# Optimization experiments

Measured on AMD Instinct MI355X. Metric: run time of the kernel, lower is better.

Reference implementation:

```python
import jax, jax.numpy as jnp
import numpy as np

N_NODES = 100000
N_EDGES = 3200000
D_IN = 128
D_OUT = 128


def setup_inputs() -> dict:
    key = jax.random.key(0)
    k1, k2, k3, k4, k5, k6 = jax.random.split(key, 6)
    features = jax.random.normal(k1, (N_NODES, D_IN), dtype=jnp.float32)
    norm = jax.random.uniform(k2, (N_EDGES, 1), dtype=jnp.float32)
    src = jax.random.randint(k3, (N_EDGES,), 0, N_NODES)
    dst = jax.random.randint(k4, (N_EDGES,), 0, N_NODES)
    weight = jax.random.normal(k5, (D_OUT, D_IN), dtype=jnp.float32) * (1.0 / np.sqrt(D_IN))
    bias = jax.random.normal(k6, (D_OUT,), dtype=jnp.float32) * 0.01
    return {"features": features, "norm": norm, "src": src, "dst": dst,
            "weight": weight, "bias": bias}


def reference(features, norm, src, dst, weight, bias):
    # message: per-edge gather of src features scaled by edge norm  [E, D_IN]
    msg = norm * features[src]
    # reduce: segment-sum into destination nodes  [N, D_IN]
    h_neigh = jax.ops.segment_sum(msg, dst, num_segments=N_NODES)
    # dense linear (nn.Linear: x @ W^T + b)  [N, D_OUT]
    return h_neigh @ weight.T + bias
```

## Files before the change

### kernel.cpp

```cpp
#include <hip/hip_runtime.h>


#define NN    100000
#define NE    3200000
#define D     128
#define NBKT2 1563
#define NTILE 6250

typedef __attribute__((ext_vector_type(8))) short bf16x8;
typedef __attribute__((ext_vector_type(4))) float f32x4;

static __device__ __forceinline__ unsigned short f2bf(float x) {
  unsigned u = __float_as_uint(x);
  u += 0x7FFFu + ((u >> 16) & 1u);
  return (unsigned short)(u >> 16);
}

static __device__ __forceinline__ void fmix8(float* acc, uint4 q, float nr) {
  asm("v_fma_mix_f32 %0, %1, %2, %0 op_sel:[0,0,0] op_sel_hi:[1,0,0]"
      : "+v"(acc[0]) : "v"(q.x), "v"(nr));
  asm("v_fma_mix_f32 %0, %1, %2, %0 op_sel:[1,0,0] op_sel_hi:[1,0,0]"
      : "+v"(acc[1]) : "v"(q.x), "v"(nr));
  asm("v_fma_mix_f32 %0, %1, %2, %0 op_sel:[0,0,0] op_sel_hi:[1,0,0]"
      : "+v"(acc[2]) : "v"(q.y), "v"(nr));
  asm("v_fma_mix_f32 %0, %1, %2, %0 op_sel:[1,0,0] op_sel_hi:[1,0,0]"
      : "+v"(acc[3]) : "v"(q.y), "v"(nr));
  asm("v_fma_mix_f32 %0, %1, %2, %0 op_sel:[0,0,0] op_sel_hi:[1,0,0]"
      : "+v"(acc[4]) : "v"(q.z), "v"(nr));
  asm("v_fma_mix_f32 %0, %1, %2, %0 op_sel:[1,0,0] op_sel_hi:[1,0,0]"
      : "+v"(acc[5]) : "v"(q.z), "v"(nr));
  asm("v_fma_mix_f32 %0, %1, %2, %0 op_sel:[0,0,0] op_sel_hi:[1,0,0]"
      : "+v"(acc[6]) : "v"(q.w), "v"(nr));
  asm("v_fma_mix_f32 %0, %1, %2, %0 op_sel:[1,0,0] op_sel_hi:[1,0,0]"
      : "+v"(acc[7]) : "v"(q.w), "v"(nr));
}

__global__ __launch_bounds__(256) void cvtw_kernel(
    const float* __restrict__ w, unsigned short* __restrict__ wfrag) {
  const int i = blockIdx.x * 256 + threadIdx.x;
  const int c = i >> 7, k = i & 127;
  const int pos = ((((c >> 4) << 2) + (k >> 5)) * 64 +
                   (((k >> 3) & 3) << 4) + (c & 15)) * 8 + (k & 7);
  wfrag[pos] = f2bf(w[i]);
}

__global__ __launch_bounds__(256) void gemm_kernel(
    const float* __restrict__ f, const unsigned short* __restrict__ wfrag,
    unsigned short* __restrict__ gh) {
  const int wv = blockIdx.x * 4 + (threadIdx.x >> 6);
  if (wv >= NTILE) return;
  const int lane = threadIdx.x & 63;
  const int mrow = lane & 15;
  const int q = lane >> 4;
  const long node = (long)wv * 16 + mrow;
  const float* fr = f + node * D + q * 8;

  bf16x8 a[4];
#pragma unroll
  for (int ks = 0; ks < 4; ++ks) {
    const float4 lo = *(const float4*)(fr + ks * 32);
    const float4 hi = *(const float4*)(fr + ks * 32 + 4);
    union { bf16x8 v; unsigned short u[8]; } pa;
    pa.u[0] = f2bf(lo.x); pa.u[1] = f2bf(lo.y);
    pa.u[2] = f2bf(lo.z); pa.u[3] = f2bf(lo.w);
    pa.u[4] = f2bf(hi.x); pa.u[5] = f2bf(hi.y);
    pa.u[6] = f2bf(hi.z); pa.u[7] = f2bf(hi.w);
    a[ks] = pa.v;
  }

  const long nbase = (long)wv * 16 + (q << 2);
#pragma unroll
  for (int tc = 0; tc < 8; ++tc) {
    f32x4 acc = {0.f, 0.f, 0.f, 0.f};
#pragma unroll
    for (int ks = 0; ks < 4; ++ks) {
      const bf16x8 b =
          *(const bf16x8*)(wfrag + (((tc << 2) + ks) * 64 + lane) * 8);
      acc = __builtin_amdgcn_mfma_f32_16x16x32_bf16(a[ks], b, acc, 0, 0, 0);
    }
    const int c = (tc << 4) + mrow;
#pragma unroll
    for (int r = 0; r < 4; ++r) {
      union { _Float16 h; unsigned short u; } cv;
      cv.h = (_Float16)acc[r];
      gh[(nbase + r) * D + c] = cv.u;
    }
  }
}

__global__ __launch_bounds__(256) void hist_kernel(const int* __restrict__ dst,
                                                   int* __restrict__ gcnt) {
  __shared__ int h[NBKT2];
  const int t = threadIdx.x;
  for (int b = t; b < NBKT2; b += 256) h[b] = 0;
  __syncthreads();
  const int base = blockIdx.x * 4096;
#pragma unroll
  for (int i = 0; i < 16; ++i) {
    int e = base + i * 256 + t;
    if (e < NE) atomicAdd(&h[dst[e] >> 6], 1);
  }
  __syncthreads();
  for (int b = t; b < NBKT2; b += 256)
    if (h[b]) atomicAdd(&gcnt[b], h[b]);
}

__global__ __launch_bounds__(1024) void scan_kernel(const int* __restrict__ gcnt,
                                                    int* __restrict__ bstart,
                                                    int* __restrict__ cur,
                                                    int* __restrict__ row_ptr) {
  __shared__ int s[2048];
  const int t = threadIdx.x;
  s[t] = (t < NBKT2) ? gcnt[t] : 0;
  s[t + 1024] = (t + 1024 < NBKT2) ? gcnt[t + 1024] : 0;
  __syncthreads();
  if (t < 64) {
    int part = 0;
#pragma unroll
    for (int i = 0; i < 32; ++i) part += s[(t << 5) + i];
    int inc = part;
#pragma unroll
    for (int off = 1; off < 64; off <<= 1) {
      int x = __shfl_up(inc, off, 64);
      if (t >= off) inc += x;
    }
    int run = inc - part;
#pragma unroll
    for (int i = 0; i < 32; ++i) {
      int idx = (t << 5) + i;
      int v = s[idx];
      s[idx] = run;
      run += v;
    }
  }
  __syncthreads();
  if (t < NBKT2) { bstart[t] = s[t]; cur[t] = s[t]; }
  if (t + 1024 < NBKT2) { bstart[t + 1024] = s[t + 1024]; cur[t + 1024] = s[t + 1024]; }
  if (t == 0) { bstart[NBKT2] = NE; row_ptr[NN] = NE; }
}

__global__ __launch_bounds__(512) void bin_kernel(
    const int* __restrict__ src, const int* __restrict__ dst,
    const float* __restrict__ norm, int* __restrict__ cur,
    int2* __restrict__ bufA) {
  __shared__ int bcnt[NBKT2];
  __shared__ int bbase[NBKT2];
  const int t = threadIdx.x;
  for (int b = t; b < NBKT2; b += 512) bcnt[b] = 0;
  __syncthreads();
  const int base = blockIdx.x * 16384;
#pragma unroll
  for (int i = 0; i < 32; ++i) {
    int e = base + i * 512 + t;
    if (e < NE) atomicAdd(&bcnt[dst[e] >> 6], 1);
  }
  __syncthreads();
  for (int b = t; b < NBKT2; b += 512) {
    int c = bcnt[b];
    if (c) bbase[b] = atomicAdd(&cur[b], c);
    bcnt[b] = 0;
  }
  __syncthreads();
#pragma unroll
  for (int i = 0; i < 32; ++i) {
    int e = base + i * 512 + t;
    if (e < NE) {
      int d = dst[e];
      int b = d >> 6;
      int r = atomicAdd(&bcnt[b], 1);
      int2 m;
      m.x = src[e] | ((d & 63) << 24);
      m.y = __float_as_int(norm[e]);
      bufA[bbase[b] + r] = m;
    }
  }
}

__global__ __launch_bounds__(256) void sort_kernel(
    const int2* __restrict__ bufA, const int* __restrict__ bstart,
    int2* __restrict__ bufB, int* __restrict__ row_ptr) {
  __shared__ int lcnt[64];
  __shared__ int lbase[64];
  const int b = blockIdx.x;
  const int t = threadIdx.x;
  const int beg = bstart[b];
  const int end = bstart[b + 1];
  if (t < 64) lcnt[t] = 0;
  __syncthreads();
  for (int e = beg + t; e < end; e += 256) {
    int2 m = bufA[e];
    atomicAdd(&lcnt[(m.x >> 24) & 63], 1);
  }
  __syncthreads();
  if (t < 64) {
    int v = lcnt[t];
    int inc = v;
#pragma unroll
    for (int off = 1; off < 64; off <<= 1) {
      int x = __shfl_up(inc, off, 64);
      if (t >= off) inc += x;
    }
    int ex = inc - v;
    lbase[t] = ex;
    int n = (b << 6) + t;
    if (n < NN) row_ptr[n] = beg + ex;
    lcnt[t] = 0;
  }
  __syncthreads();
  for (int e = beg + t; e < end; e += 256) {
    int2 m = bufA[e];
    int nl = (m.x >> 24) & 63;
    int r = atomicAdd(&lcnt[nl], 1);
    int2 o;
    o.x = m.x & 0xFFFFFF;
    o.y = m.y;
    bufB[beg + lbase[nl] + r] = o;
  }
}

__global__ __launch_bounds__(256) void pull_kernel(
    const unsigned short* __restrict__ gh, const int* __restrict__ row_ptr,
    const int2* __restrict__ bufB, const float* __restrict__ bias,
    float* __restrict__ out) {
  const int n = blockIdx.x * 4 + (threadIdx.x >> 6);
  if (n >= NN) return;
  const int lane = threadIdx.x & 63;
  const int s = lane & 15;
  const int g = lane >> 4;
  const int beg = row_ptr[n];
  const int end = row_ptr[n + 1];

  float acc[8] = {0.f, 0.f, 0.f, 0.f, 0.f, 0.f, 0.f, 0.f};

  if (beg < end) {
    const char* gbase = (const char*)gh;
    const unsigned soff = (unsigned)(s << 4);
    const int last = end - 1;
    int e0 = beg;
    int2 mA0 = bufB[min(e0 + g, last)];
    int2 mB0 = bufB[min(e0 + 4 + g, last)];
    uint4 qA0 = *(const uint4*)(gbase + (((unsigned)mA0.x << 8) + soff));
    uint4 qB0 = *(const uint4*)(gbase + (((unsigned)mB0.x << 8) + soff));
    int2 mA1 = bufB[min(e0 + 8 + g, last)];
    int2 mB1 = bufB[min(e0 + 12 + g, last)];
    while (e0 + 8 < end) {
      const int2 mA2 = bufB[min(e0 + 16 + g, last)];
      const int2 mB2 = bufB[min(e0 + 20 + g, last)];
      const uint4 qA1 =
          *(const uint4*)(gbase + (((unsigned)mA1.x << 8) + soff));
      const uint4 qB1 =
          *(const uint4*)(gbase + (((unsigned)mB1.x << 8) + soff));
      fmix8(acc, qA0, __int_as_float(mA0.y));
      fmix8(acc, qB0, __int_as_float(mB0.y));
      mA0 = mA1; mB0 = mB1;
      mA1 = mA2; mB1 = mB2;
      qA0 = qA1; qB0 = qB1;
      e0 += 8;
    }
    const float nrA = (e0 + g < end) ? __int_as_float(mA0.y) : 0.f;
    const float nrB = (e0 + 4 + g < end) ? __int_as_float(mB0.y) : 0.f;
    fmix8(acc, qA0, nrA);
    fmix8(acc, qB0, nrB);
  }

#pragma unroll
  for (int k = 0; k < 8; ++k) {
    acc[k] += __shfl_xor(acc[k], 16, 64);
    acc[k] += __shfl_xor(acc[k], 32, 64);
  }
  if (g < 2) {
    const bool hi = (g == 1);
    const float r0 = hi ? acc[4] : acc[0];
    const float r1 = hi ? acc[5] : acc[1];
    const float r2 = hi ? acc[6] : acc[2];
    const float r3 = hi ? acc[7] : acc[3];
    const int cb = (s << 3) + (g << 2);
    const float4 b4 = *(const float4*)(bias + cb);
    float4 r;
    r.x = r0 + b4.x;
    r.y = r1 + b4.y;
    r.z = r2 + b4.z;
    r.w = r3 + b4.w;
    *(float4*)(out + (long)n * D + cb) = r;
  }
}

__global__ __launch_bounds__(256) void gemm_f32_kernel(
    const float* __restrict__ f, const float* __restrict__ w,
    float* __restrict__ g) {
  __shared__ float wlds[D * D];
  const int t = threadIdx.x;
  for (int i = t; i < D * D; i += 256) {
    int c = i >> 7, k = i & 127;
    wlds[(c << 7) + (k ^ (c & 31))] = w[i];
  }
  __syncthreads();
  const int c = t & 127;
  const int cx = c & 31;
  const int cbase = c << 7;
  const int jbase = __builtin_amdgcn_readfirstlane((t >> 7) << 3);
  const long nb = (long)blockIdx.x * 16 + jbase;
  const float* __restrict__ frow = f + nb * D;
  float acc[8] = {0.f, 0.f, 0.f, 0.f, 0.f, 0.f, 0.f, 0.f};
#pragma unroll 4
  for (int k = 0; k < D; ++k) {
    float wv = wlds[cbase + (k ^ cx)];
#pragma unroll
    for (int j = 0; j < 8; ++j) acc[j] += frow[j * D + k] * wv;
  }
#pragma unroll
  for (int j = 0; j < 8; ++j) g[(nb + j) * D + c] = acc[j];
}

__global__ __launch_bounds__(256) void init_kernel(
    const float* __restrict__ bias, float4* __restrict__ out) {
  const int i = blockIdx.x * 256 + threadIdx.x;
  const float4* b4 = (const float4*)bias;
  out[i] = b4[i & 31];
}

__global__ __launch_bounds__(256) void scatter_kernel(
    const float* __restrict__ g, const float* __restrict__ norm,
    const int* __restrict__ src, const int* __restrict__ dst,
    float* __restrict__ out) {
  const long tid = (long)blockIdx.x * 256 + threadIdx.x;
  const int e = (int)(tid >> 5);
  if (e >= NE) return;
  const int ch = (int)(tid & 31) << 2;
  const int s = src[e];
  const int d = dst[e];
  const float nr = norm[e];
  const float4 gv = *(const float4*)(g + (long)s * D + ch);
  float* op = out + (long)d * D + ch;
  unsafeAtomicAdd(op + 0, nr * gv.x);
  unsafeAtomicAdd(op + 1, nr * gv.y);
  unsafeAtomicAdd(op + 2, nr * gv.z);
  unsafeAtomicAdd(op + 3, nr * gv.w);
}

extern "C" void kernel_launch(void* const* d_in, const int* in_sizes, int n_in,
                              void* d_out, int out_size, void* d_ws,
                              size_t ws_size, hipStream_t stream) {
  const float* features = (const float*)d_in[0];
  const float* norm     = (const float*)d_in[1];
  const int*   src      = (const int*)d_in[2];
  const int*   dst      = (const int*)d_in[3];
  const float* weight   = (const float*)d_in[4];
  const float* bias     = (const float*)d_in[5];
  float* out = (float*)d_out;

  char* ws = (char*)d_ws;
  unsigned short* gh    = (unsigned short*)ws;
  int2* bufA    = (int2*)(ws + 25600000);
  int2* bufB    = (int2*)(ws + 51200000);
  int*  row_ptr = (int*)(ws + 76800000);
  int*  gcnt    = (int*)(ws + 77200008);
  int*  bstart  = (int*)(ws + 77206264);
  int*  cur     = (int*)(ws + 77212524);
  unsigned short* wfrag = (unsigned short*)(ws + 77218784);
  const size_t need = 77251552;

  if (ws_size >= need) {
    hipMemsetAsync(gcnt, 0, NBKT2 * sizeof(int), stream);
    hipLaunchKernelGGL(cvtw_kernel, dim3(64), dim3(256), 0, stream,
                       weight, wfrag);
    hipLaunchKernelGGL(gemm_kernel, dim3((NTILE + 3) / 4), dim3(256), 0,
                       stream, features, wfrag, gh);
    hipLaunchKernelGGL(hist_kernel, dim3((NE + 4095) / 4096), dim3(256), 0,
                       stream, dst, gcnt);
    hipLaunchKernelGGL(scan_kernel, dim3(1), dim3(1024), 0, stream,
                       gcnt, bstart, cur, row_ptr);
    hipLaunchKernelGGL(bin_kernel, dim3((NE + 16383) / 16384), dim3(512), 0,
                       stream, src, dst, norm, cur, bufA);
    hipLaunchKernelGGL(sort_kernel, dim3(NBKT2), dim3(256), 0, stream,
                       bufA, bstart, bufB, row_ptr);
    hipLaunchKernelGGL(pull_kernel, dim3((NN + 3) / 4), dim3(256), 0, stream,
                       gh, row_ptr, bufB, bias, out);
  } else {
    float* g = (float*)ws;
    hipLaunchKernelGGL(gemm_f32_kernel, dim3(NN / 16), dim3(256), 0, stream,
                       features, weight, g);
    hipLaunchKernelGGL(init_kernel, dim3((NN * D / 4) / 256), dim3(256), 0,
                       stream, bias, (float4*)out);
    hipLaunchKernelGGL(scatter_kernel, dim3((long)NE * 32 / 256), dim3(256), 0,
                       stream, g, norm, src, dst, out);
  }
}
```

Before: 392.7 us.

## Replace two-level bucket sort with direct per-node counting sort via global atomics

Swaps the bucketed histogram, bin and local-sort pipeline for a per-node histogram built with global atomics, a single-block 100k-entry scan, and a placement kernel that scatters each edge straight to its final CSR slot using an atomic on its destination counter. This drops the intermediate bufA pass and the sort kernel, cutting memory traffic and kernel launches. In exchange it relies on heavy global atomic contention, scatters 8-byte writes at random addresses, and makes the order of edges within a node nondeterministic. The scan now runs on one block over 100k entries, which may serialize.

```diff
diff --git a/kernel.cpp b/kernel.cpp
--- a/kernel.cpp
+++ b/kernel.cpp
@@ -4,7 +4,6 @@
 #define NN    100000
 #define NE    3200000
 #define D     128
-#define NBKT2 1563
 #define NTILE 6250
 
 typedef __attribute__((ext_vector_type(8))) short bf16x8;
@@ -88,134 +87,105 @@
   }
 }
 
-__global__ __launch_bounds__(256) void hist_kernel(const int* __restrict__ dst,
-                                                   int* __restrict__ gcnt) {
-  __shared__ int h[NBKT2];
+__global__ __launch_bounds__(256) void histn_kernel(const int* __restrict__ dst,
+                                                    int* __restrict__ cur) {
+  const int i = blockIdx.x * 256 + threadIdx.x;
+  const int4 d = ((const int4*)dst)[i];
+  atomicAdd(&cur[d.x], 1);
+  atomicAdd(&cur[d.y], 1);
+  atomicAdd(&cur[d.z], 1);
+  atomicAdd(&cur[d.w], 1);
+}
+
+__global__ __launch_bounds__(1024) void scan100k_kernel(
+    int* __restrict__ cur, int* __restrict__ row_ptr) {
+  __shared__ int wsum[16];
   const int t = threadIdx.x;
-  for (int b = t; b < NBKT2; b += 256) h[b] = 0;
+  const int w = t >> 6, lane = t & 63;
+  const int wbeg = w * 6400;
+
+  int tot = 0;
+  for (int base = wbeg; base < wbeg + 6400; base += 256) {
+    const int idx = base + lane * 4;
+    int4 v = {0, 0, 0, 0};
+    if (idx + 3 < NN) v = *(const int4*)(cur + idx);
+    else {
+      if (idx + 0 < NN) v.x = cur[idx + 0];
+      if (idx + 1 < NN) v.y = cur[idx + 1];
+      if (idx + 2 < NN) v.z = cur[idx + 2];
+      if (idx + 3 < NN) v.w = cur[idx + 3];
+    }
+    tot += v.x + v.y + v.z + v.w;
+  }
+#pragma unroll
+  for (int off = 1; off < 64; off <<= 1) tot += __shfl_xor(tot, off, 64);
+  if (lane == 0) wsum[w] = tot;
   __syncthreads();
-  const int base = blockIdx.x * 4096;
-#pragma unroll
-  for (int i = 0; i < 16; ++i) {
-    int e = base + i * 256 + t;
-    if (e < NE) atomicAdd(&h[dst[e] >> 6], 1);
+  if (w == 0 && lane < 16) {
+    const int v = wsum[lane];
+    int inc = v;
+#pragma unroll
+    for (int off = 1; off < 16; off <<= 1) {
+      int x = __shfl_up(inc, off, 64);
+      if (lane >= off) inc += x;
+    }
+    wsum[lane] = inc - v;
   }
   __syncthreads();
-  for (int b = t; b < NBKT2; b += 256)
-    if (h[b]) atomicAdd(&gcnt[b], h[b]);
-}
-
-__global__ __launch_bounds__(1024) void scan_kernel(const int* __restrict__ gcnt,
-                                                    int* __restrict__ bstart,
-                                                    int* __restrict__ cur,
-                                                    int* __restrict__ row_ptr) {
-  __shared__ int s[2048];
-  const int t = threadIdx.x;
-  s[t] = (t < NBKT2) ? gcnt[t] : 0;
-  s[t + 1024] = (t + 1024 < NBKT2) ? gcnt[t + 1024] : 0;
-  __syncthreads();
-  if (t < 64) {
-    int part = 0;
-#pragma unroll
-    for (int i = 0; i < 32; ++i) part += s[(t << 5) + i];
-    int inc = part;
+
+  int run = wsum[w];
+  for (int base = wbeg; base < wbeg + 6400; base += 256) {
+    const int idx = base + lane * 4;
+    int4 v = {0, 0, 0, 0};
+    const bool full = (idx + 3 < NN);
+    if (full) v = *(const int4*)(cur + idx);
+    else {
+      if (idx + 0 < NN) v.x = cur[idx + 0];
+      if (idx + 1 < NN) v.y = cur[idx + 1];
+      if (idx + 2 < NN) v.z = cur[idx + 2];
+      if (idx + 3 < NN) v.w = cur[idx + 3];
+    }
+    const int s = v.x + v.y + v.z + v.w;
+    int inc = s;
 #pragma unroll
     for (int off = 1; off < 64; off <<= 1) {
       int x = __shfl_up(inc, off, 64);
-      if (t >= off) inc += x;
-    }
-    int run = inc - part;
-#pragma unroll
-    for (int i = 0; i < 32; ++i) {
-      int idx = (t << 5) + i;
-      int v = s[idx];
-      s[idx] = run;
-      run += v;
-    }
-  }
-  __syncthreads();
-  if (t < NBKT2) { bstart[t] = s[t]; cur[t] = s[t]; }
-  if (t + 1024 < NBKT2) { bstart[t + 1024] = s[t + 1024]; cur[t + 1024] = s[t + 1024]; }
-  if (t == 0) { bstart[NBKT2] = NE; row_ptr[NN] = NE; }
-}
-
-__global__ __launch_bounds__(512) void bin_kernel(
+      if (lane >= off) inc += x;
+    }
+    const int ex = run + inc - s;
+    int4 o;
+    o.x = ex;
+    o.y = ex + v.x;
+    o.z = ex + v.x + v.y;
+    o.w = ex + v.x + v.y + v.z;
+    if (full) {
+      *(int4*)(cur + idx) = o;
+      *(int4*)(row_ptr + idx) = o;
+    } else {
+      if (idx + 0 < NN) { cur[idx + 0] = o.x; row_ptr[idx + 0] = o.x; }
+      if (idx + 1 < NN) { cur[idx + 1] = o.y; row_ptr[idx + 1] = o.y; }
+      if (idx + 2 < NN) { cur[idx + 2] = o.z; row_ptr[idx + 2] = o.z; }
+      if (idx + 3 < NN) { cur[idx + 3] = o.w; row_ptr[idx + 3] = o.w; }
+    }
+    run += __shfl(inc, 63, 64);
+  }
+  if (t == 0) row_ptr[NN] = NE;
+}
+
+__global__ __launch_bounds__(256) void place_kernel(
     const int* __restrict__ src, const int* __restrict__ dst,
     const float* __restrict__ norm, int* __restrict__ cur,
-    int2* __restrict__ bufA) {
-  __shared__ int bcnt[NBKT2];
-  __shared__ int bbase[NBKT2];
-  const int t = threadIdx.x;
-  for (int b = t; b < NBKT2; b += 512) bcnt[b] = 0;
-  __syncthreads();
-  const int base = blockIdx.x * 16384;
-#pragma unroll
-  for (int i = 0; i < 32; ++i) {
-    int e = base + i * 512 + t;
-    if (e < NE) atomicAdd(&bcnt[dst[e] >> 6], 1);
-  }
-  __syncthreads();
-  for (int b = t; b < NBKT2; b += 512) {
-    int c = bcnt[b];
-    if (c) bbase[b] = atomicAdd(&cur[b], c);
-    bcnt[b] = 0;
-  }
-  __syncthreads();
-#pragma unroll
-  for (int i = 0; i < 32; ++i) {
-    int e = base + i * 512 + t;
-    if (e < NE) {
-      int d = dst[e];
-      int b = d >> 6;
-      int r = atomicAdd(&bcnt[b], 1);
-      int2 m;
-      m.x = src[e] | ((d & 63) << 24);
-      m.y = __float_as_int(norm[e]);
-      bufA[bbase[b] + r] = m;
-    }
-  }
-}
-
-__global__ __launch_bounds__(256) void sort_kernel(
-    const int2* __restrict__ bufA, const int* __restrict__ bstart,
-    int2* __restrict__ bufB, int* __restrict__ row_ptr) {
-  __shared__ int lcnt[64];
-  __shared__ int lbase[64];
-  const int b = blockIdx.x;
-  const int t = threadIdx.x;
-  const int beg = bstart[b];
-  const int end = bstart[b + 1];
-  if (t < 64) lcnt[t] = 0;
-  __syncthreads();
-  for (int e = beg + t; e < end; e += 256) {
-    int2 m = bufA[e];
-    atomicAdd(&lcnt[(m.x >> 24) & 63], 1);
-  }
-  __syncthreads();
-  if (t < 64) {
-    int v = lcnt[t];
-    int inc = v;
-#pragma unroll
-    for (int off = 1; off < 64; off <<= 1) {
-      int x = __shfl_up(inc, off, 64);
-      if (t >= off) inc += x;
-    }
-    int ex = inc - v;
-    lbase[t] = ex;
-    int n = (b << 6) + t;
-    if (n < NN) row_ptr[n] = beg + ex;
-    lcnt[t] = 0;
-  }
-  __syncthreads();
-  for (int e = beg + t; e < end; e += 256) {
-    int2 m = bufA[e];
-    int nl = (m.x >> 24) & 63;
-    int r = atomicAdd(&lcnt[nl], 1);
-    int2 o;
-    o.x = m.x & 0xFFFFFF;
-    o.y = m.y;
-    bufB[beg + lbase[nl] + r] = o;
-  }
+    int2* __restrict__ bufB) {
+  const int i = blockIdx.x * 256 + threadIdx.x;
+  const int4 s = ((const int4*)src)[i];
+  const int4 d = ((const int4*)dst)[i];
+  const float4 nr = ((const float4*)norm)[i];
+  int2 m;
+  int r;
+  r = atomicAdd(&cur[d.x], 1); m.x = s.x; m.y = __float_as_int(nr.x); bufB[r] = m;
+  r = atomicAdd(&cur[d.y], 1); m.x = s.y; m.y = __float_as_int(nr.y); bufB[r] = m;
+  r = atomicAdd(&cur[d.z], 1); m.x = s.z; m.y = __float_as_int(nr.z); bufB[r] = m;
+  r = atomicAdd(&cur[d.w], 1); m.x = s.w; m.y = __float_as_int(nr.w); bufB[r] = m;
 }
 
 __global__ __launch_bounds__(256) void pull_kernel(
@@ -351,29 +321,24 @@
 
   char* ws = (char*)d_ws;
   unsigned short* gh    = (unsigned short*)ws;
-  int2* bufA    = (int2*)(ws + 25600000);
-  int2* bufB    = (int2*)(ws + 51200000);
-  int*  row_ptr = (int*)(ws + 76800000);
-  int*  gcnt    = (int*)(ws + 77200008);
-  int*  bstart  = (int*)(ws + 77206264);
-  int*  cur     = (int*)(ws + 77212524);
-  unsigned short* wfrag = (unsigned short*)(ws + 77218784);
-  const size_t need = 77251552;
+  int2* bufB    = (int2*)(ws + 25600000);
+  int*  row_ptr = (int*)(ws + 51200000);
+  int*  cur     = (int*)(ws + 51600016);
+  unsigned short* wfrag = (unsigned short*)(ws + 52000016);
+  const size_t need = 52032784;
 
   if (ws_size >= need) {
-    hipMemsetAsync(gcnt, 0, NBKT2 * sizeof(int), stream);
+    hipMemsetAsync(cur, 0, NN * sizeof(int), stream);
     hipLaunchKernelGGL(cvtw_kernel, dim3(64), dim3(256), 0, stream,
                        weight, wfrag);
     hipLaunchKernelGGL(gemm_kernel, dim3((NTILE + 3) / 4), dim3(256), 0,
                        stream, features, wfrag, gh);
-    hipLaunchKernelGGL(hist_kernel, dim3((NE + 4095) / 4096), dim3(256), 0,
-                       stream, dst, gcnt);
-    hipLaunchKernelGGL(scan_kernel, dim3(1), dim3(1024), 0, stream,
-                       gcnt, bstart, cur, row_ptr);
-    hipLaunchKernelGGL(bin_kernel, dim3((NE + 16383) / 16384), dim3(512), 0,
-                       stream, src, dst, norm, cur, bufA);
-    hipLaunchKernelGGL(sort_kernel, dim3(NBKT2), dim3(256), 0, stream,
-                       bufA, bstart, bufB, row_ptr);
+    hipLaunchKernelGGL(histn_kernel, dim3(NE / 1024), dim3(256), 0, stream,
+                       dst, cur);
+    hipLaunchKernelGGL(scan100k_kernel, dim3(1), dim3(1024), 0, stream,
+                       cur, row_ptr);
+    hipLaunchKernelGGL(place_kernel, dim3(NE / 1024), dim3(256), 0, stream,
+                       src, dst, norm, cur, bufB);
     hipLaunchKernelGGL(pull_kernel, dim3((NN + 3) / 4), dim3(256), 0, stream,
                        gh, row_ptr, bufB, bias, out);
   } else {
```

New measurement: 628.9 us. 1.6x slower.

## Fuse histogram into GEMM launch and coarsen counting-sort buckets to 256 nodes

Applied to the files above, without the earlier changes.

Folds the destination histogram into the GEMM kernel as extra blocks so it runs concurrently with the feature transform. Bucket width grows from 64 to 256 nodes, which cuts the bucket count to 391, and the histogram and binning kernels read inputs as int4 with replicated shared-memory counters to reduce atomic contention. The sort kernel now handles 256 nodes per bucket with a two-level scan. Larger buckets mean fewer global atomics and launches, but the sort blocks become larger and less balanced.

```diff
diff --git a/kernel.cpp b/kernel.cpp
--- a/kernel.cpp
+++ b/kernel.cpp
@@ -4,8 +4,11 @@
 #define NN    100000
 #define NE    3200000
 #define D     128
-#define NBKT2 1563
+#define NBKT  391
+#define NI4   800000
 #define NTILE 6250
+#define GB    1563
+#define HB    782
 
 typedef __attribute__((ext_vector_type(8))) short bf16x8;
 typedef __attribute__((ext_vector_type(4))) float f32x4;
@@ -44,9 +47,36 @@
   wfrag[pos] = f2bf(w[i]);
 }
 
-__global__ __launch_bounds__(256) void gemm_kernel(
+__global__ __launch_bounds__(256) void gemmhist_kernel(
     const float* __restrict__ f, const unsigned short* __restrict__ wfrag,
-    unsigned short* __restrict__ gh) {
+    unsigned short* __restrict__ gh, const int* __restrict__ dst,
+    int* __restrict__ gcnt) {
+  __shared__ int h[4][NBKT];
+  if (blockIdx.x >= GB) {
+    const int t = threadIdx.x;
+    for (int i = t; i < 4 * NBKT; i += 256) ((int*)h)[i] = 0;
+    __syncthreads();
+    const int i4base = (blockIdx.x - GB) * 1024;
+    const int rep = t & 3;
+#pragma unroll
+    for (int i = 0; i < 4; ++i) {
+      const int idx = i4base + i * 256 + t;
+      if (idx < NI4) {
+        const int4 d = ((const int4*)dst)[idx];
+        atomicAdd(&h[rep][d.x >> 8], 1);
+        atomicAdd(&h[rep][d.y >> 8], 1);
+        atomicAdd(&h[rep][d.z >> 8], 1);
+        atomicAdd(&h[rep][d.w >> 8], 1);
+      }
+    }
+    __syncthreads();
+    for (int b = t; b < NBKT; b += 256) {
+      const int v = h[0][b] + h[1][b] + h[2][b] + h[3][b];
+      if (v) atomicAdd(&gcnt[b], v);
+    }
+    return;
+  }
+
   const int wv = blockIdx.x * 4 + (threadIdx.x >> 6);
   if (wv >= NTILE) return;
   const int lane = threadIdx.x & 63;
@@ -81,38 +111,21 @@
     const int c = (tc << 4) + mrow;
 #pragma unroll
     for (int r = 0; r < 4; ++r) {
-      union { _Float16 h; unsigned short u; } cv;
-      cv.h = (_Float16)acc[r];
+      union { _Float16 hh; unsigned short u; } cv;
+      cv.hh = (_Float16)acc[r];
       gh[(nbase + r) * D + c] = cv.u;
     }
   }
-}
-
-__global__ __launch_bounds__(256) void hist_kernel(const int* __restrict__ dst,
-                                                   int* __restrict__ gcnt) {
-  __shared__ int h[NBKT2];
-  const int t = threadIdx.x;
-  for (int b = t; b < NBKT2; b += 256) h[b] = 0;
-  __syncthreads();
-  const int base = blockIdx.x * 4096;
-#pragma unroll
-  for (int i = 0; i < 16; ++i) {
-    int e = base + i * 256 + t;
-    if (e < NE) atomicAdd(&h[dst[e] >> 6], 1);
-  }
-  __syncthreads();
-  for (int b = t; b < NBKT2; b += 256)
-    if (h[b]) atomicAdd(&gcnt[b], h[b]);
 }
 
 __global__ __launch_bounds__(1024) void scan_kernel(const int* __restrict__ gcnt,
                                                     int* __restrict__ bstart,
-                                                    int* __restrict__ cur,
+                                                    int* __restrict__ cur_b,
                                                     int* __restrict__ row_ptr) {
   __shared__ int s[2048];
   const int t = threadIdx.x;
-  s[t] = (t < NBKT2) ? gcnt[t] : 0;
-  s[t + 1024] = (t + 1024 < NBKT2) ? gcnt[t + 1024] : 0;
+  s[t] = (t < NBKT) ? gcnt[t] : 0;
+  s[t + 1024] = 0;
   __syncthreads();
   if (t < 64) {
     int part = 0;
@@ -134,85 +147,112 @@
     }
   }
   __syncthreads();
-  if (t < NBKT2) { bstart[t] = s[t]; cur[t] = s[t]; }
-  if (t + 1024 < NBKT2) { bstart[t + 1024] = s[t + 1024]; cur[t + 1024] = s[t + 1024]; }
-  if (t == 0) { bstart[NBKT2] = NE; row_ptr[NN] = NE; }
-}
-
-__global__ __launch_bounds__(512) void bin_kernel(
+  if (t < NBKT) { bstart[t] = s[t]; cur_b[t] = s[t]; }
+  if (t == 0) { bstart[NBKT] = NE; row_ptr[NN] = NE; }
+}
+
+__global__ __launch_bounds__(1024) void bin_kernel(
     const int* __restrict__ src, const int* __restrict__ dst,
-    const float* __restrict__ norm, int* __restrict__ cur,
+    const float* __restrict__ norm, int* __restrict__ cur_b,
     int2* __restrict__ bufA) {
-  __shared__ int bcnt[NBKT2];
-  __shared__ int bbase[NBKT2];
+  __shared__ int bcnt[4][NBKT];
+  __shared__ int bbase[NBKT];
+  __shared__ int brank[NBKT];
   const int t = threadIdx.x;
-  for (int b = t; b < NBKT2; b += 512) bcnt[b] = 0;
-  __syncthreads();
-  const int base = blockIdx.x * 16384;
-#pragma unroll
-  for (int i = 0; i < 32; ++i) {
-    int e = base + i * 512 + t;
-    if (e < NE) atomicAdd(&bcnt[dst[e] >> 6], 1);
-  }
-  __syncthreads();
-  for (int b = t; b < NBKT2; b += 512) {
-    int c = bcnt[b];
-    if (c) bbase[b] = atomicAdd(&cur[b], c);
-    bcnt[b] = 0;
-  }
-  __syncthreads();
-#pragma unroll
-  for (int i = 0; i < 32; ++i) {
-    int e = base + i * 512 + t;
-    if (e < NE) {
-      int d = dst[e];
-      int b = d >> 6;
-      int r = atomicAdd(&bcnt[b], 1);
-      int2 m;
-      m.x = src[e] | ((d & 63) << 24);
-      m.y = __float_as_int(norm[e]);
-      bufA[bbase[b] + r] = m;
-    }
-  }
-}
-
-__global__ __launch_bounds__(256) void sort_kernel(
+  for (int i = t; i < 4 * NBKT; i += 1024) ((int*)bcnt)[i] = 0;
+  if (t < NBKT) brank[t] = 0;
+  __syncthreads();
+  const int i4base = blockIdx.x * 4096;
+  const int rep = t & 3;
+#pragma unroll
+  for (int i = 0; i < 4; ++i) {
+    const int idx = i4base + i * 1024 + t;
+    if (idx < NI4) {
+      const int4 d = ((const int4*)dst)[idx];
+      atomicAdd(&bcnt[rep][d.x >> 8], 1);
+      atomicAdd(&bcnt[rep][d.y >> 8], 1);
+      atomicAdd(&bcnt[rep][d.z >> 8], 1);
+      atomicAdd(&bcnt[rep][d.w >> 8], 1);
+    }
+  }
+  __syncthreads();
+  if (t < NBKT) {
+    const int c = bcnt[0][t] + bcnt[1][t] + bcnt[2][t] + bcnt[3][t];
+    if (c) bbase[t] = atomicAdd(&cur_b[t], c);
+  }
+  __syncthreads();
+#pragma unroll
+  for (int i = 0; i < 4; ++i) {
+    const int idx = i4base + i * 1024 + t;
+    if (idx < NI4) {
+      const int4 s = ((const int4*)src)[idx];
+      const int4 d = ((const int4*)dst)[idx];
+      const float4 nr = ((const float4*)norm)[idx];
+      int bb, r; int2 m;
+      bb = d.x >> 8; r = atomicAdd(&brank[bb], 1);
+      m.x = s.x | ((d.x & 255) << 17); m.y = __float_as_int(nr.x);
+      bufA[bbase[bb] + r] = m;
+      bb = d.y >> 8; r = atomicAdd(&brank[bb], 1);
+      m.x = s.y | ((d.y & 255) << 17); m.y = __float_as_int(nr.y);
+      bufA[bbase[bb] + r] = m;
+      bb = d.z >> 8; r = atomicAdd(&brank[bb], 1);
+      m.x = s.z | ((d.z & 255) << 17); m.y = __float_as_int(nr.z);
+      bufA[bbase[bb] + r] = m;
+      bb = d.w >> 8; r = atomicAdd(&brank[bb], 1);
+      m.x = s.w | ((d.w & 255) << 17); m.y = __float_as_int(nr.w);
+      bufA[bbase[bb] + r] = m;
+    }
+  }
+}
+
+__global__ __launch_bounds__(512) void sort_kernel(
     const int2* __restrict__ bufA, const int* __restrict__ bstart,
     int2* __restrict__ bufB, int* __restrict__ row_ptr) {
-  __shared__ int lcnt[64];
-  __shared__ int lbase[64];
+  __shared__ int lcnt[256];
+  __shared__ int lbase[256];
+  __shared__ int wtot[4];
   const int b = blockIdx.x;
   const int t = threadIdx.x;
   const int beg = bstart[b];
   const int end = bstart[b + 1];
-  if (t < 64) lcnt[t] = 0;
-  __syncthreads();
-  for (int e = beg + t; e < end; e += 256) {
-    int2 m = bufA[e];
-    atomicAdd(&lcnt[(m.x >> 24) & 63], 1);
-  }
-  __syncthreads();
-  if (t < 64) {
-    int v = lcnt[t];
-    int inc = v;
+  if (t < 256) lcnt[t] = 0;
+  __syncthreads();
+  for (int e = beg + t; e < end; e += 512)
+    atomicAdd(&lcnt[(bufA[e].x >> 17) & 255], 1);
+  __syncthreads();
+  int v = 0, inc = 0;
+  const int lane = t & 63;
+  if (t < 256) {
+    v = lcnt[t];
+    inc = v;
 #pragma unroll
     for (int off = 1; off < 64; off <<= 1) {
       int x = __shfl_up(inc, off, 64);
-      if (t >= off) inc += x;
-    }
-    int ex = inc - v;
+      if (lane >= off) inc += x;
+    }
+    if (lane == 63) wtot[t >> 6] = inc;
+  }
+  __syncthreads();
+  if (t == 0) {
+    int run = 0;
+#pragma unroll
+    for (int i = 0; i < 4; ++i) { int x = wtot[i]; wtot[i] = run; run += x; }
+  }
+  __syncthreads();
+  if (t < 256) {
+    const int ex = wtot[t >> 6] + inc - v;
     lbase[t] = ex;
-    int n = (b << 6) + t;
+    const int n = (b << 8) + t;
     if (n < NN) row_ptr[n] = beg + ex;
     lcnt[t] = 0;
   }
   __syncthreads();
-  for (int e = beg + t; e < end; e += 256) {
-    int2 m = bufA[e];
-    int nl = (m.x >> 24) & 63;
-    int r = atomicAdd(&lcnt[nl], 1);
+  for (int e = beg + t; e < end; e += 512) {
+    const int2 m = bufA[e];
+    const int nl = (m.x >> 17) & 255;
+    const int r = atomicAdd(&lcnt[nl], 1);
     int2 o;
-    o.x = m.x & 0xFFFFFF;
+    o.x = m.x & 0x1FFFF;
     o.y = m.y;
     bufB[beg + lbase[nl] + r] = o;
   }
@@ -354,25 +394,23 @@
   int2* bufA    = (int2*)(ws + 25600000);
   int2* bufB    = (int2*)(ws + 51200000);
   int*  row_ptr = (int*)(ws + 76800000);
-  int*  gcnt    = (int*)(ws + 77200008);
-  int*  bstart  = (int*)(ws + 77206264);
-  int*  cur     = (int*)(ws + 77212524);
-  unsigned short* wfrag = (unsigned short*)(ws + 77218784);
-  const size_t need = 77251552;
+  int*  gcnt    = (int*)(ws + 77200016);
+  int*  bstart  = (int*)(ws + 77201584);
+  int*  cur_b   = (int*)(ws + 77203152);
+  unsigned short* wfrag = (unsigned short*)(ws + 77204720);
+  const size_t need = 77237488;
 
   if (ws_size >= need) {
-    hipMemsetAsync(gcnt, 0, NBKT2 * sizeof(int), stream);
+    hipMemsetAsync(gcnt, 0, NBKT * sizeof(int), stream);
     hipLaunchKernelGGL(cvtw_kernel, dim3(64), dim3(256), 0, stream,
                        weight, wfrag);
-    hipLaunchKernelGGL(gemm_kernel, dim3((NTILE + 3) / 4), dim3(256), 0,
-                       stream, features, wfrag, gh);
-    hipLaunchKernelGGL(hist_kernel, dim3((NE + 4095) / 4096), dim3(256), 0,
-                       stream, dst, gcnt);
+    hipLaunchKernelGGL(gemmhist_kernel, dim3(GB + HB), dim3(256), 0, stream,
+                       features, wfrag, gh, dst, gcnt);
     hipLaunchKernelGGL(scan_kernel, dim3(1), dim3(1024), 0, stream,
-                       gcnt, bstart, cur, row_ptr);
-    hipLaunchKernelGGL(bin_kernel, dim3((NE + 16383) / 16384), dim3(512), 0,
-                       stream, src, dst, norm, cur, bufA);
-    hipLaunchKernelGGL(sort_kernel, dim3(NBKT2), dim3(256), 0, stream,
+                       gcnt, bstart, cur_b, row_ptr);
+    hipLaunchKernelGGL(bin_kernel, dim3((NI4 + 4095) / 4096), dim3(1024), 0,
+                       stream, src, dst, norm, cur_b, bufA);
+    hipLaunchKernelGGL(sort_kernel, dim3(NBKT), dim3(512), 0, stream,
                        bufA, bstart, bufB, row_ptr);
     hipLaunchKernelGGL(pull_kernel, dim3((NN + 3) / 4), dim3(256), 0, stream,
                        gh, row_ptr, bufB, bias, out);
```

Measured after the change: 340.6 us. 13.3% less time.
